# Performance work log

Hardware: AMD Instinct MI355X
Metric: run time of the kernel (lower is better)

Reference implementation:

```python
import jax, jax.numpy as jnp
import numpy as np

B, N, NE = 16, 96, 256
ATOM, EDIM, HID, LAT, HEADS = 128, 16, 128, 128, 4
HD = LAT // HEADS
RBF, CUT, ZEMB, MAXZ = 16, 5.0, 32, 100
MUL0_IN, MUL1_IN = 64, 32      # irreps_node = 64x0e + 32x1o (dim 160)
MUL0_OUT, MUL1_OUT = 32, 16    # out irreps  = 32x0e + 16x1o (dim 80)
NODE_DIM = MUL0_IN + 3 * MUL1_IN
OUT_DIM = MUL0_OUT + 3 * MUL1_OUT
E_ATT = 1024
WNUM = MUL0_IN*MUL0_OUT + MUL0_IN*MUL1_OUT + MUL1_IN*MUL1_OUT + MUL1_IN*MUL0_OUT  # 4608


def _mlp3(x, w1, b1, w2, b2, w3, b3):
    x = jax.nn.silu(x @ w1 + b1)
    x = jax.nn.silu(x @ w2 + b2)
    return x @ w3 + b3


def setup_inputs() -> dict:
    key = jax.random.key(0)
    ks = jax.random.split(key, 40)
    s = 0.05  # scale params so deep MLP activations stay numerically sane
    d = {}
    d['h'] = jax.random.normal(ks[0], (B, N, ATOM), jnp.float32)
    d['h_full'] = jax.random.normal(ks[1], (B, N, NODE_DIM), jnp.float32)
    d['e_feat'] = jax.random.normal(ks[2], (NE, EDIM), jnp.float32)
    d['att_dist'] = jax.random.uniform(ks[3], (E_ATT,), jnp.float32)
    d['att_vec'] = jax.random.normal(ks[4], (E_ATT, 3), jnp.float32)
    d['z_emb_table'] = jax.random.normal(ks[5], (MAXZ + 1, ZEMB), jnp.float32) * s
    d['rw1'] = jax.random.normal(ks[6], (ZEMB + 1 + RBF, HID), jnp.float32) * s
    d['rb1'] = jnp.zeros((HID,), jnp.float32)
    d['rw2'] = jax.random.normal(ks[7], (HID, WNUM), jnp.float32) * s
    d['rb2'] = jnp.zeros((WNUM,), jnp.float32)
    d['ew1'] = jax.random.normal(ks[8], (EDIM, HID), jnp.float32) * s
    d['eb1'] = jnp.zeros((HID,), jnp.float32)
    d['ew2'] = jax.random.normal(ks[9], (HID, MUL0_OUT + MUL1_OUT), jnp.float32) * s
    d['eb2'] = jnp.zeros((MUL0_OUT + MUL1_OUT,), jnp.float32)
    d['qw1'] = jax.random.normal(ks[10], (ATOM + EDIM, HID), jnp.float32) * s
    d['qb1'] = jnp.zeros((HID,), jnp.float32)
    d['qw2'] = jax.random.normal(ks[11], (HID, HID), jnp.float32) * s
    d['qb2'] = jnp.zeros((HID,), jnp.float32)
    d['qw3'] = jax.random.normal(ks[12], (HID, LAT), jnp.float32) * s
    d['qb3'] = jnp.zeros((LAT,), jnp.float32)
    d['kw1'] = jax.random.normal(ks[13], (ATOM + ZEMB + 1 + RBF, HID), jnp.float32) * s
    d['kb1'] = jnp.zeros((HID,), jnp.float32)
    d['kw2'] = jax.random.normal(ks[14], (HID, HID), jnp.float32) * s
    d['kb2'] = jnp.zeros((HID,), jnp.float32)
    d['kw3'] = jax.random.normal(ks[15], (HID, LAT), jnp.float32) * s
    d['kb3'] = jnp.zeros((LAT,), jnp.float32)
    d['ow1'] = jax.random.normal(ks[16], (MUL0_OUT + MUL1_OUT, HID), jnp.float32) * s
    d['ob1'] = jnp.zeros((HID,), jnp.float32)
    d['ow2'] = jax.random.normal(ks[17], (HID, HID), jnp.float32) * s
    d['ob2'] = jnp.zeros((HID,), jnp.float32)
    d['ow3'] = jax.random.normal(ks[18], (HID, LAT), jnp.float32) * s
    d['ob3'] = jnp.zeros((LAT,), jnp.float32)
    d['z'] = jax.random.randint(ks[19], (B, N), 0, MAXZ)
    d['mask'] = jnp.ones((B, N), bool)
    d['absorber_index'] = jax.random.randint(ks[20], (B,), 0, N)
    d['att_dst'] = jnp.arange(E_ATT)  # unique flat indices into B*N
    return d


def reference(h, h_full, e_feat, att_dist, att_vec, z_emb_table,
              rw1, rb1, rw2, rb2, ew1, eb1, ew2, eb2,
              qw1, qb1, qw2, qb2, qw3, qb3,
              kw1, kb1, kw2, kb2, kw3, kb3,
              ow1, ob1, ow2, ob2, ow3, ob3,
              z, mask, absorber_index, att_dst):
    Bz, Na, Hd = h.shape
    F = Bz * Na
    nE = e_feat.shape[0]
    # scatter edge data into flat (B*N) atom slots
    am_flat = jnp.zeros((F,), bool).at[att_dst].set(True)
    d_flat = jnp.zeros((F,), h.dtype).at[att_dst].set(att_dist)
    v_flat = jnp.zeros((F, 3), h.dtype).at[att_dst].set(att_vec)
    att_mask = am_flat.reshape(Bz, Na) & mask
    # spherical harmonics (lmax=1, component normalization): Y0 = 1, Y1 = sqrt(3)*unit_vec
    un = v_flat / jnp.maximum(jnp.linalg.norm(v_flat, axis=-1, keepdims=True), 1e-8)
    y1 = jnp.sqrt(3.0) * un
    # Gaussian RBF on absorber->atom distance
    mu = jnp.linspace(0.0, CUT, RBF)
    delta = CUT / (RBF - 1)
    rbf = jnp.exp(-(d_flat[:, None] - mu) ** 2 / (2.0 * delta * delta))  # (F, RBF)
    zr = z_emb_table[z]                      # (B, N, ZEMB)
    zr_flat = zr.reshape(F, -1)
    is_abs = jnp.zeros((Bz, Na), h.dtype).at[jnp.arange(Bz), absorber_index].set(1.0)
    # radial MLP -> per-edge tensor-product weights
    w_in = jnp.concatenate([zr_flat, is_abs.reshape(F, 1), rbf], -1)
    tpw = jax.nn.silu(w_in @ rw1 + rb1) @ rw2 + rb2  # (F, WNUM)
    s1 = MUL0_IN * MUL0_OUT
    s2 = s1 + MUL0_IN * MUL1_OUT
    s3 = s2 + MUL1_IN * MUL1_OUT
    w00 = tpw[:, :s1].reshape(F, MUL0_IN, MUL0_OUT)   # 0e x 0e -> 0e
    w01 = tpw[:, s1:s2].reshape(F, MUL0_IN, MUL1_OUT) # 0e x 1o -> 1o
    w10 = tpw[:, s2:s3].reshape(F, MUL1_IN, MUL1_OUT) # 1o x 0e -> 1o
    w11 = tpw[:, s3:].reshape(F, MUL1_IN, MUL0_OUT)   # 1o x 1o -> 0e
    hf = h_full.reshape(F, -1)
    x0 = hf[:, :MUL0_IN]
    x1 = hf[:, MUL0_IN:].reshape(F, MUL1_IN, 3)
    alpha = 1.0 / jnp.sqrt(jnp.float32(MUL0_IN + MUL1_IN))  # path fan-in normalization
    c = 1.0 / jnp.sqrt(3.0)                                  # wigner-3j coeff for l=1 couplings
    out0 = alpha * (jnp.einsum('fi,fio->fo', x0, w00)
                    + c * jnp.einsum('fim,fm,fio->fo', x1, y1, w11))
    out1 = alpha * c * (jnp.einsum('fi,fm,fio->fom', x0, y1, w01)
                        + jnp.einsum('fim,fio->fom', x1, w10))
    v_irrep = jnp.concatenate([out0, out1.reshape(F, 3 * MUL1_OUT)], -1)  # (F, OUT_DIM)
    # cosine cutoff envelope + edge mask
    env = jnp.where(d_flat < CUT, 0.5 * (jnp.cos(jnp.pi * d_flat / CUT) + 1.0), 0.0)
    v_irrep = v_irrep * (am_flat.astype(h.dtype) * env)[:, None]
    # energy-conditioned per-irrep-channel modulation
    gates = jax.nn.silu(e_feat @ ew1 + eb1) @ ew2 + eb2  # (nE, 48)
    g_exp = jnp.concatenate([gates[:, :MUL0_OUT],
                             jnp.repeat(gates[:, MUL0_OUT:], 3, axis=-1)], -1)  # (nE, OUT_DIM)
    v_mod = (v_irrep[:, None, :] * g_exp[None]).reshape(Bz, Na, nE, OUT_DIM)
    # invariant multi-head scoring
    h_abs = h[jnp.arange(Bz), absorber_index]  # (B, H)
    q_in = jnp.concatenate([jnp.broadcast_to(h_abs[:, None], (Bz, nE, Hd)),
                            jnp.broadcast_to(e_feat[None], (Bz, nE, EDIM))], -1)
    q = _mlp3(q_in, qw1, qb1, qw2, qb2, qw3, qb3)  # (B, nE, LAT)
    atom_static = jnp.concatenate([h, zr, is_abs[..., None], rbf.reshape(Bz, Na, RBF)], -1)
    k = _mlp3(atom_static, kw1, kb1, kw2, kb2, kw3, kb3)  # (B, N, LAT)
    qh = q.reshape(Bz, nE, HEADS, HD)
    kh = k.reshape(Bz, Na, HEADS, HD)
    scores = (jnp.einsum('behd,bnhd->benh', qh, kh) * (HD ** -0.5)).mean(-1)  # (B, nE, N)
    m = att_mask[:, None, :]
    scores = jnp.where(m, scores, -1e9)
    attn = jax.nn.softmax(scores, axis=2) * m.astype(h.dtype)
    attn = attn / jnp.maximum(attn.sum(2, keepdims=True), 1e-8)
    out_irrep = jnp.einsum('ben,bnec->bec', attn, v_mod)  # (B, nE, OUT_DIM)
    # invariants: scalars + vector norms
    scal = out_irrep[..., :MUL0_OUT]
    vec = out_irrep[..., MUL0_OUT:].reshape(Bz, nE, MUL1_OUT, 3)
    inv = jnp.concatenate([scal, jnp.sqrt(jnp.sum(vec * vec, -1) + 1e-12)], -1)
    return _mlp3(inv, ow1, ob1, ow2, ob2, ow3, ob3)  # (B, nE, LAT)
```

## Files before the change

### kernel.cpp

```cpp
#include <hip/hip_runtime.h>
#include <hip/hip_fp16.h>
#include <math.h>

#define BB 16
#define NN 96
#define NE 256
#define FF (BB*NN)
#define ATOM 128
#define EDIM 16
#define HID 128
#define LAT 128
#define RBFN 16
#define CUTOFF 5.0f
#define ZEMB 32
#define E_ATT 1024
#define M0I 64
#define M1I 32
#define M0O 32
#define M1O 16
#define NODE_DIM 160
#define OUT_DIM 80
#define INVD 48
#define WNUM 4608
#define SEG1 2048
#define SEG2 3072
#define SEG3 3584

#define NODE_BLKS (FF/4)
#define EC_BLKS 16
#define HABS_BLKS 2
#define GATE_BLKS 16
#define TRANS_BLKS 144
#define STAGE1_BLKS (NODE_BLKS + EC_BLKS + HABS_BLKS + GATE_BLKS + TRANS_BLKS)

#define MFMA_BLKS (36*16)
#define MQ_BLKS (MFMA_BLKS + 512)

typedef _Float16 half8_t __attribute__((ext_vector_type(8)));
typedef float float4v __attribute__((ext_vector_type(4)));

__device__ __forceinline__ float silu_f(float x) { return x / (1.0f + expf(-x)); }

__global__ __launch_bounds__(1024) void k_prep(
    const int* __restrict__ att_dst, const float* __restrict__ att_dist,
    const float* __restrict__ att_vec,
    int* __restrict__ inv, float* __restrict__ y1E, float* __restrict__ envE)
{
    int t = threadIdx.x;
    inv[t] = -1;
    if (t < FF - 1024) inv[1024 + t] = -1;
    {
        float d = att_dist[t];
        envE[t] = (d < CUTOFF) ? 0.5f*(cosf(3.14159265358979323846f*d/CUTOFF) + 1.0f) : 0.0f;
        float vx = att_vec[3*t], vy = att_vec[3*t+1], vz = att_vec[3*t+2];
        float nrm = sqrtf(vx*vx + vy*vy + vz*vz);
        float is = 1.0f / fmaxf(nrm, 1e-8f);
        const float s3 = 1.7320508075688772f;
        y1E[3*t]   = s3*vx*is;
        y1E[3*t+1] = s3*vy*is;
        y1E[3*t+2] = s3*vz*is;
    }
    __syncthreads();
    inv[att_dst[t]] = t;
}

__global__ __launch_bounds__(256) void k_stage1(
    const float* __restrict__ h, const float* __restrict__ z_emb, const int* __restrict__ z,
    const int* __restrict__ absorber, const float* __restrict__ e_feat,
    const int* __restrict__ inv, const float* __restrict__ att_dist,
    const float* __restrict__ rw1, const float* __restrict__ rb1,
    const float* __restrict__ kw1, const float* __restrict__ kb1,
    const float* __restrict__ kw2, const float* __restrict__ kb2,
    const float* __restrict__ kw3, const float* __restrict__ kb3,
    const float* __restrict__ qw1,
    const float* __restrict__ ew1, const float* __restrict__ eb1,
    const float* __restrict__ ew2, const float* __restrict__ eb2,
    const float* __restrict__ rw2,
    __half* __restrict__ hiddenH, float* __restrict__ kmatw,
    float* __restrict__ ecw, float* __restrict__ habs1w, float* __restrict__ gexp,
    __half* __restrict__ rw2T)
{
    __shared__ float smem[3488];
    int blk = blockIdx.x;
    int t = threadIdx.x;

    if (blk < NODE_BLKS) {
        float (*sin1)[184] = (float(*)[184])smem;
        float (*l1S)[128]  = (float(*)[128])(smem + 736);
        float (*l2S)[128]  = (float(*)[128])(smem + 736 + 512);
        int f0 = blk * 4;
        {
            int n = t >> 6, i2 = t & 63;
            float2 hv = *(const float2*)&h[(f0 + n)*ATOM + i2*2];
            sin1[n][i2*2] = hv.x; sin1[n][i2*2 + 1] = hv.y;
        }
        if (t < 128) {
            int n = t >> 5, j = t & 31;
            sin1[n][ATOM + j] = z_emb[z[f0 + n]*ZEMB + j];
        }
        if (t < 64) {
            int n = t >> 4, j = t & 15;
            int e = inv[f0 + n];
            float d = ((unsigned)e < E_ATT) ? att_dist[e] : 0.0f;
            const float delta = CUTOFF / (RBFN - 1);
            float diff = d - j*delta;
            sin1[n][ATOM + ZEMB + 1 + j] = expf(-diff*diff / (2.0f*delta*delta));
        }
        if (t < 4) {
            int f = f0 + t;
            int b = f / NN, nn = f - b*NN;
            sin1[t][ATOM + ZEMB] = (absorber[b] == nn) ? 1.0f : 0.0f;
        }
        __syncthreads();
        int n = t >> 6;
        int c2 = (t & 63) * 2;
        int e = inv[f0 + n];
        bool att_ = ((unsigned)e < E_ATT);
        if (att_) {
            float2 a0 = *(const float2*)&rb1[c2];
            float2 a1 = make_float2(0.f, 0.f);
            #pragma unroll 8
            for (int i = 0; i < 48; i += 2) {
                float x0v = sin1[n][ATOM + i], x1v = sin1[n][ATOM + i + 1];
                float2 w0 = *(const float2*)&rw1[i*HID + c2];
                float2 w1 = *(const float2*)&rw1[(i+1)*HID + c2];
                a0.x += x0v*w0.x; a0.y += x0v*w0.y;
                a1.x += x1v*w1.x; a1.y += x1v*w1.y;
            }
            {
                float x0v = sin1[n][ATOM + 48];
                float2 w0 = *(const float2*)&rw1[48*HID + c2];
                a0.x += x0v*w0.x; a0.y += x0v*w0.y;
            }
            *(__half2*)&hiddenH[e*HID + c2] =
                __floats2half2_rn(silu_f(a0.x + a1.x), silu_f(a0.y + a1.y));
        }
        {
            float2 a0 = *(const float2*)&kb1[c2];
            float2 a1 = make_float2(0.f, 0.f);
            #pragma unroll 8
            for (int i = 0; i < 176; i += 2) {
                float x0v = sin1[n][i], x1v = sin1[n][i + 1];
                float2 w0 = *(const float2*)&kw1[i*HID + c2];
                float2 w1 = *(const float2*)&kw1[(i+1)*HID + c2];
                a0.x += x0v*w0.x; a0.y += x0v*w0.y;
                a1.x += x1v*w1.x; a1.y += x1v*w1.y;
            }
            {
                float x0v = sin1[n][176];
                float2 w0 = *(const float2*)&kw1[176*HID + c2];
                a0.x += x0v*w0.x; a0.y += x0v*w0.y;
            }
            l1S[n][c2] = silu_f(a0.x + a1.x); l1S[n][c2+1] = silu_f(a0.y + a1.y);
        }
        __syncthreads();
        {
            float2 a0 = *(const float2*)&kb2[c2];
            float2 a1 = make_float2(0.f, 0.f);
            #pragma unroll 8
            for (int i = 0; i < HID; i += 2) {
                float x0v = l1S[n][i], x1v = l1S[n][i + 1];
                float2 w0 = *(const float2*)&kw2[i*HID + c2];
                float2 w1 = *(const float2*)&kw2[(i+1)*HID + c2];
                a0.x += x0v*w0.x; a0.y += x0v*w0.y;
                a1.x += x1v*w1.x; a1.y += x1v*w1.y;
            }
            l2S[n][c2] = silu_f(a0.x + a1.x); l2S[n][c2+1] = silu_f(a0.y + a1.y);
        }
        __syncthreads();
        {
            float2 a0 = *(const float2*)&kb3[c2];
            float2 a1 = make_float2(0.f, 0.f);
            #pragma unroll 8
            for (int i = 0; i < HID; i += 2) {
                float x0v = l2S[n][i], x1v = l2S[n][i + 1];
                float2 w0 = *(const float2*)&kw3[i*HID + c2];
                float2 w1 = *(const float2*)&kw3[(i+1)*HID + c2];
                a0.x += x0v*w0.x; a0.y += x0v*w0.y;
                a1.x += x1v*w1.x; a1.y += x1v*w1.y;
            }
            float2 o; o.x = a0.x + a1.x; o.y = a0.y + a1.y;
            *(float2*)&kmatw[(f0 + n)*HID + c2] = o;
        }
    } else if (blk < NODE_BLKS + EC_BLKS) {
        float (*ef)[16] = (float(*)[16])smem;
        int e0 = (blk - NODE_BLKS) * 16;
        { int e = t >> 4, i = t & 15; ef[e][i] = e_feat[(e0 + e)*EDIM + i]; }
        __syncthreads();
        int r = t >> 4, c0 = (t & 15)*8;
        float4 a0 = make_float4(0,0,0,0), a1 = a0;
        #pragma unroll
        for (int i = 0; i < EDIM; i++) {
            float a = ef[r][i];
            float4 w0 = *(const float4*)&qw1[(ATOM + i)*HID + c0];
            float4 w1 = *(const float4*)&qw1[(ATOM + i)*HID + c0 + 4];
            a0.x += a*w0.x; a0.y += a*w0.y; a0.z += a*w0.z; a0.w += a*w0.w;
            a1.x += a*w1.x; a1.y += a*w1.y; a1.z += a*w1.z; a1.w += a*w1.w;
        }
        *(float4*)&ecw[(e0 + r)*HID + c0] = a0;
        *(float4*)&ecw[(e0 + r)*HID + c0 + 4] = a1;
    } else if (blk < NODE_BLKS + EC_BLKS + HABS_BLKS) {
        float (*hr)[128] = (float(*)[128])smem;
        int b0 = (blk - NODE_BLKS - EC_BLKS) * 8;
        {
            int r = t >> 5, i4 = t & 31;
            int b = b0 + r;
            int a = absorber[b];
            *(float4*)&hr[r][i4*4] = *(const float4*)&h[(b*NN + a)*ATOM + i4*4];
        }
        __syncthreads();
        int r = t >> 5, c0 = (t & 31)*4;
        float4 a0 = make_float4(0,0,0,0), a1 = a0;
        #pragma unroll 8
        for (int i = 0; i < ATOM; i += 2) {
            float x0v = hr[r][i], x1v = hr[r][i+1];
            float4 w0 = *(const float4*)&qw1[i*HID + c0];
            float4 w1 = *(const float4*)&qw1[(i+1)*HID + c0];
            a0.x += x0v*w0.x; a0.y += x0v*w0.y; a0.z += x0v*w0.z; a0.w += x0v*w0.w;
            a1.x += x1v*w1.x; a1.y += x1v*w1.y; a1.z += x1v*w1.z; a1.w += x1v*w1.w;
        }
        float4 o;
        o.x = a0.x + a1.x; o.y = a0.y + a1.y; o.z = a0.z + a1.z; o.w = a0.w + a1.w;
        *(float4*)&habs1w[(b0 + r)*HID + c0] = o;
    } else if (blk < NODE_BLKS + EC_BLKS + HABS_BLKS + GATE_BLKS) {
        float (*ef)[16]   = (float(*)[16])smem;
        float (*l1g)[128] = (float(*)[128])(smem + 256);
        float (*gg)[48]   = (float(*)[48])(smem + 256 + 2048);
        int e0 = (blk - NODE_BLKS - EC_BLKS - HABS_BLKS) * 16;
        { int e = t >> 4, i = t & 15; ef[e][i] = e_feat[(e0 + e)*EDIM + i]; }
        __syncthreads();
        int r = t >> 4, c0 = (t & 15)*8;
        {
            float4 a0 = *(const float4*)&eb1[c0];
            float4 a1 = *(const float4*)&eb1[c0 + 4];
            #pragma unroll
            for (int i = 0; i < EDIM; i++) {
                float a = ef[r][i];
                float4 w0 = *(const float4*)&ew1[i*HID + c0];
                float4 w1 = *(const float4*)&ew1[i*HID + c0 + 4];
                a0.x += a*w0.x; a0.y += a*w0.y; a0.z += a*w0.z; a0.w += a*w0.w;
                a1.x += a*w1.x; a1.y += a*w1.y; a1.z += a*w1.z; a1.w += a*w1.w;
            }
            l1g[r][c0]   = silu_f(a0.x); l1g[r][c0+1] = silu_f(a0.y);
            l1g[r][c0+2] = silu_f(a0.z); l1g[r][c0+3] = silu_f(a0.w);
            l1g[r][c0+4] = silu_f(a1.x); l1g[r][c0+5] = silu_f(a1.y);
            l1g[r][c0+6] = silu_f(a1.z); l1g[r][c0+7] = silu_f(a1.w);
        }
        __syncthreads();
        for (int u = t; u < 16*48; u += 256) {
            int e = u / 48, j = u - 48*(u/48);
            float acc = eb2[j];
            #pragma unroll 4
            for (int i = 0; i < HID; i++) acc += l1g[e][i]*ew2[i*48 + j];
            gg[e][j] = acc;
        }
        __syncthreads();
        for (int u = t; u < 16*80; u += 256) {
            int e = u / 80, cc = u - 80*(u/80);
            gexp[(e0 + e)*OUT_DIM + cc] = (cc < M0O) ? gg[e][cc] : gg[e][M0O + (cc - M0O)/3];
        }
    } else {
        __half* lds = (__half*)smem;
        int tb = blk - (NODE_BLKS + EC_BLKS + HABS_BLKS + GATE_BLKS);
        int nt = tb % 72, kt = tb / 72;
        int n0 = nt*64, k0 = kt*64;
        for (int p = 0; p < 16; p++) {
            int idx = t + 256*p;
            int kk = idx >> 6, nn = idx & 63;
            lds[nn*66 + kk] = __float2half(rw2[(k0+kk)*WNUM + n0+nn]);
        }
        __syncthreads();
        for (int p = 0; p < 16; p++) {
            int idx = t + 256*p;
            int nn = idx >> 6, kk = idx & 63;
            rw2T[(n0+nn)*HID + k0+kk] = lds[nn*66 + kk];
        }
    }
}

__global__ __launch_bounds__(256) void k_mq(
    const __half* __restrict__ hiddenH, const __half* __restrict__ rw2T,
    const float* __restrict__ rb2,
    const float* __restrict__ habs1, const float* __restrict__ ec, const float* __restrict__ qb1,
    const float* __restrict__ qw2, const float* __restrict__ qb2,
    const float* __restrict__ qw3, const float* __restrict__ qb3,
    __half* __restrict__ tpwE, float* __restrict__ qmat)
{
    __shared__ __align__(16) char smemraw[17408];
    int blk = blockIdx.x;
    int t = threadIdx.x;
    if (blk < MFMA_BLKS) {
        int colTile = blk % 36;
        int rowGrp  = blk / 36;
        int wv = t >> 6;
        int lane = t & 63;
        int m0 = (rowGrp*4 + wv) * 16;
        int n0 = colTile * 128;
        int mrow = lane & 15, quad = lane >> 4;
        __half* cS = (__half*)smemraw + wv * (16*136);
        const _Float16* hp = (const _Float16*)hiddenH + (m0 + mrow)*HID + quad*8;
        half8_t af[4];
        #pragma unroll
        for (int kc = 0; kc < 4; kc++) af[kc] = *(const half8_t*)(hp + kc*32);
        #pragma unroll
        for (int nt = 0; nt < 8; nt++) {
            const _Float16* bp = (const _Float16*)rw2T + (n0 + nt*16 + mrow)*HID + quad*8;
            float4v acc = {0.f, 0.f, 0.f, 0.f};
            #pragma unroll
            for (int kc = 0; kc < 4; kc++) {
                half8_t bf = *(const half8_t*)(bp + kc*32);
                acc = __builtin_amdgcn_mfma_f32_16x16x32_f16(af[kc], bf, acc, 0, 0, 0);
            }
            float bias = rb2[n0 + nt*16 + mrow];
            #pragma unroll
            for (int r = 0; r < 4; r++)
                cS[(quad*4 + r)*136 + nt*16 + mrow] = __float2half(acc[r] + bias);
        }
        #pragma unroll
        for (int p = 0; p < 4; p++) {
            int chunk = lane + 64*p;
            int row = chunk >> 4, c8 = (chunk & 15)*8;
            float4 v = *(float4*)&cS[row*136 + c8];
            *(float4*)&tpwE[(long)(m0 + row)*WNUM + n0 + c8] = v;
        }
    } else {
        float* l1S = (float*)smemraw;
        float* l2S = (float*)smemraw + 1024;
        int r0 = (blk - MFMA_BLKS) * 8;
        for (int p = 0; p < 4; p++) {
            int idx = t + 256*p;
            int rr = idx >> 7, i = idx & 127;
            int be = r0 + rr; int b = be >> 8; int e = be & 255;
            l1S[rr*128 + i] = silu_f(habs1[b*HID + i] + ec[e*HID + i] + qb1[i]);
        }
        __syncthreads();
        int r = t >> 5, c0 = (t & 31)*4;
        {
            float4 a0 = *(const float4*)&qb2[c0];
            float4 a1 = make_float4(0,0,0,0);
            #pragma unroll 8
            for (int i = 0; i < HID; i += 2) {
                float x0v = l1S[r*128 + i], x1v = l1S[r*128 + i+1];
                float4 w0 = *(const float4*)&qw2[i*HID + c0];
                float4 w1 = *(const float4*)&qw2[(i+1)*HID + c0];
                a0.x += x0v*w0.x; a0.y += x0v*w0.y; a0.z += x0v*w0.z; a0.w += x0v*w0.w;
                a1.x += x1v*w1.x; a1.y += x1v*w1.y; a1.z += x1v*w1.z; a1.w += x1v*w1.w;
            }
            l2S[r*128 + c0]   = silu_f(a0.x + a1.x); l2S[r*128 + c0+1] = silu_f(a0.y + a1.y);
            l2S[r*128 + c0+2] = silu_f(a0.z + a1.z); l2S[r*128 + c0+3] = silu_f(a0.w + a1.w);
        }
        __syncthreads();
        {
            float4 a0 = *(const float4*)&qb3[c0];
            float4 a1 = make_float4(0,0,0,0);
            #pragma unroll 8
            for (int i = 0; i < HID; i += 2) {
                float x0v = l2S[r*128 + i], x1v = l2S[r*128 + i+1];
                float4 w0 = *(const float4*)&qw3[i*HID + c0];
                float4 w1 = *(const float4*)&qw3[(i+1)*HID + c0];
                a0.x += x0v*w0.x; a0.y += x0v*w0.y; a0.z += x0v*w0.z; a0.w += x0v*w0.w;
                a1.x += x1v*w1.x; a1.y += x1v*w1.y; a1.z += x1v*w1.z; a1.w += x1v*w1.w;
            }
            float4 o;
            o.x = a0.x + a1.x; o.y = a0.y + a1.y; o.z = a0.z + a1.z; o.w = a0.w + a1.w;
            *(float4*)&qmat[(r0 + r)*LAT + c0] = o;
        }
    }
}

__global__ __launch_bounds__(256) void k_score(
    const float* __restrict__ qmat, const float* __restrict__ kmat, const int* __restrict__ inv,
    float* __restrict__ scoresW)
{
    int b  = blockIdx.x >> 3;
    int e0 = (blockIdx.x & 7) * 32;
    int t = threadIdx.x;
    __shared__ float Qs[32][132];
    __shared__ float Ks[96][132];
    __shared__ float mS[NN];

    for (int p = 0; p < 4; p++) {
        int idx = t + 256*p; int e = idx >> 5, i4 = idx & 31;
        *(float4*)&Qs[e][i4*4] = *(const float4*)&qmat[(b*NE + e0 + e)*LAT + i4*4];
    }
    for (int p = 0; p < 12; p++) {
        int idx = t + 256*p; int n = idx >> 5, i4 = idx & 31;
        *(float4*)&Ks[n][i4*4] = *(const float4*)&kmat[(b*NN + n)*LAT + i4*4];
    }
    if (t < NN) mS[t] = ((unsigned)inv[b*NN + t] < E_ATT) ? 1.0f : 0.0f;
    __syncthreads();

    int te = t >> 5;
    int tn = t & 31;
    float acc[4][3] = {};
    for (int i = 0; i < LAT; i++) {
        float bv0 = Ks[tn][i], bv1 = Ks[tn + 32][i], bv2 = Ks[tn + 64][i];
        #pragma unroll
        for (int j = 0; j < 4; j++) {
            float a = Qs[te*4 + j][i];
            acc[j][0] += a*bv0; acc[j][1] += a*bv1; acc[j][2] += a*bv2;
        }
    }
    const float scale = 0.04419417382415922f;
    #pragma unroll
    for (int j = 0; j < 4; j++)
        #pragma unroll
        for (int jj = 0; jj < 3; jj++) {
            int n = tn + 32*jj;
            float s = (mS[n] != 0.f) ? acc[j][jj]*scale : -1e9f;
            scoresW[((b*NE) + e0 + te*4 + j)*NN + n] = s;
        }
}

__global__ __launch_bounds__(256) void k_tp(
    const float* __restrict__ h_full, const __half* __restrict__ tpwE,
    const int* __restrict__ att_dst,
    const float* __restrict__ envE, const float* __restrict__ y1E,
    float* __restrict__ virr)
{
    int t = threadIdx.x;
    int sub = t >> 7, tt = t & 127;
    int e = blockIdx.x*2 + sub;
    int f = att_dst[e];
    __shared__ float x0[2][M0I];
    __shared__ float x1f[2][M1I*3];
    __shared__ float xy[2][M1I];
    __shared__ float y1s[2][3];
    const float* hf = h_full + f*NODE_DIM;
    if (tt < M0I) x0[sub][tt] = hf[tt];
    if (tt < M1I*3) x1f[sub][tt] = hf[M0I + tt];
    if (tt < 3) y1s[sub][tt] = y1E[3*e + tt];
    __syncthreads();
    if (tt < M1I) xy[sub][tt] = x1f[sub][3*tt]*y1s[sub][0] + x1f[sub][3*tt+1]*y1s[sub][1]
                              + x1f[sub][3*tt+2]*y1s[sub][2];
    __syncthreads();
    float scale = envE[e];
    const __half* w = tpwE + (long)e*WNUM;
    const float alpha = 0.10206207261596575f;
    const float cc = 0.5773502691896258f;
    if (tt < M0O) {
        float t00 = 0.f, t11 = 0.f;
        #pragma unroll 4
        for (int i = 0; i < M0I; i++) t00 += x0[sub][i]*__half2float(w[i*M0O + tt]);
        #pragma unroll 4
        for (int i = 0; i < M1I; i++) t11 += xy[sub][i]*__half2float(w[SEG3 + i*M0O + tt]);
        virr[f*OUT_DIM + tt] = alpha*(t00 + cc*t11)*scale;
    } else if (tt < M0O + 3*M1O) {
        int idx = tt - M0O; int o = idx/3, m = idx - 3*o;
        float t01 = 0.f, t10 = 0.f;
        #pragma unroll 4
        for (int i = 0; i < M0I; i++) t01 += x0[sub][i]*__half2float(w[SEG1 + i*M1O + o]);
        #pragma unroll 4
        for (int i = 0; i < M1I; i++) t10 += x1f[sub][i*3 + m]*__half2float(w[SEG2 + i*M1O + o]);
        virr[f*OUT_DIM + tt] = alpha*cc*(t01*y1s[sub][m] + t10)*scale;
    }
}

__global__ __launch_bounds__(256) void k_attf(
    const float* __restrict__ scoresW, const int* __restrict__ inv,
    const float* __restrict__ virr, const float* __restrict__ gexp,
    const float* __restrict__ ow1, const float* __restrict__ ob1,
    const float* __restrict__ ow2, const float* __restrict__ ob2,
    const float* __restrict__ ow3, const float* __restrict__ ob3,
    float* __restrict__ out)
{
    int b  = blockIdx.x >> 5;
    int e0 = (blockIdx.x & 31) * 8;
    int t = threadIdx.x;
    __shared__ float aS[8][100];
    __shared__ float gS[8][84];
    __shared__ float ocS[8][84];
    __shared__ float mS[NN];
    __shared__ float inS[8][INVD];
    __shared__ float l1S[8][HID];
    __shared__ float l2S[8][HID];

    for (int p = 0; p < 3; p++) {
        int idx = t + 256*p;
        int el = idx / NN, n = idx - NN*(idx/NN);
        aS[el][n] = scoresW[((b*NE) + e0 + el)*NN + n];
    }
    if (t < 160) {
        int el = t / 20, c4 = t - 20*(t/20);
        *(float4*)&gS[el][c4*4] = *(const float4*)&gexp[(e0 + el)*OUT_DIM + c4*4];
    }
    if (t < NN) mS[t] = ((unsigned)inv[b*NN + t] < E_ATT) ? 1.0f : 0.0f;
    __syncthreads();

    {
        int el = t >> 5;
        int ng = t & 31;
        float s0 = aS[el][ng], s1 = aS[el][ng + 32], s2 = aS[el][ng + 64];
        float m0 = mS[ng], m1 = mS[ng + 32], m2 = mS[ng + 64];
        float mx = fmaxf(s0, fmaxf(s1, s2));
        #pragma unroll
        for (int off = 1; off < 32; off <<= 1) mx = fmaxf(mx, __shfl_xor(mx, off));
        float e0v = expf(s0 - mx), e1v = expf(s1 - mx), e2v = expf(s2 - mx);
        float sm = e0v + e1v + e2v;
        #pragma unroll
        for (int off = 1; off < 32; off <<= 1) sm += __shfl_xor(sm, off);
        float r = 1.0f / sm;
        float p0 = m0*e0v*r, p1 = m1*e1v*r, p2 = m2*e2v*r;
        float ss = p0 + p1 + p2;
        #pragma unroll
        for (int off = 1; off < 32; off <<= 1) ss += __shfl_xor(ss, off);
        float is = 1.0f / fmaxf(ss, 1e-8f);
        aS[el][ng]      = p0*is;
        aS[el][ng + 32] = p1*is;
        aS[el][ng + 64] = p2*is;
    }
    __syncthreads();

    if (t < 160) {
        int el = t / 20, c4 = t - 20*(t/20);
        const float* vp = virr + (long)b*NN*OUT_DIM + c4*4;
        float4 acc = make_float4(0,0,0,0);
        #pragma unroll 4
        for (int n = 0; n < NN; n++) {
            float a = aS[el][n];
            float4 v = *(const float4*)&vp[n*OUT_DIM];
            acc.x += a*v.x; acc.y += a*v.y; acc.z += a*v.z; acc.w += a*v.w;
        }
        float4 g = *(float4*)&gS[el][c4*4];
        float4 o; o.x = acc.x*g.x; o.y = acc.y*g.y; o.z = acc.z*g.z; o.w = acc.w*g.w;
        *(float4*)&ocS[el][c4*4] = o;
    }
    __syncthreads();

    for (int u = t; u < 8*INVD; u += 256) {
        int el = u / INVD, j = u - INVD*(u/INVD);
        float val;
        if (j < M0O) val = ocS[el][j];
        else {
            int o = j - M0O;
            float x = ocS[el][M0O + 3*o], y = ocS[el][M0O + 3*o + 1], zz = ocS[el][M0O + 3*o + 2];
            val = sqrtf(x*x + y*y + zz*zz + 1e-12f);
        }
        inS[el][j] = val;
    }
    __syncthreads();

    int r = t >> 5, c0 = (t & 31)*4;
    {
        float4 a0 = *(const float4*)&ob1[c0];
        float4 a1 = make_float4(0,0,0,0);
        #pragma unroll 8
        for (int i = 0; i < INVD; i += 2) {
            float x0v = inS[r][i], x1v = inS[r][i+1];
            float4 w0 = *(const float4*)&ow1[i*HID + c0];
            float4 w1 = *(const float4*)&ow1[(i+1)*HID + c0];
            a0.x += x0v*w0.x; a0.y += x0v*w0.y; a0.z += x0v*w0.z; a0.w += x0v*w0.w;
            a1.x += x1v*w1.x; a1.y += x1v*w1.y; a1.z += x1v*w1.z; a1.w += x1v*w1.w;
        }
        l1S[r][c0]   = silu_f(a0.x + a1.x); l1S[r][c0+1] = silu_f(a0.y + a1.y);
        l1S[r][c0+2] = silu_f(a0.z + a1.z); l1S[r][c0+3] = silu_f(a0.w + a1.w);
    }
    __syncthreads();
    {
        float4 a0 = *(const float4*)&ob2[c0];
        float4 a1 = make_float4(0,0,0,0);
        #pragma unroll 8
        for (int i = 0; i < HID; i += 2) {
            float x0v = l1S[r][i], x1v = l1S[r][i+1];
            float4 w0 = *(const float4*)&ow2[i*HID + c0];
            float4 w1 = *(const float4*)&ow2[(i+1)*HID + c0];
            a0.x += x0v*w0.x; a0.y += x0v*w0.y; a0.z += x0v*w0.z; a0.w += x0v*w0.w;
            a1.x += x1v*w1.x; a1.y += x1v*w1.y; a1.z += x1v*w1.z; a1.w += x1v*w1.w;
        }
        l2S[r][c0]   = silu_f(a0.x + a1.x); l2S[r][c0+1] = silu_f(a0.y + a1.y);
        l2S[r][c0+2] = silu_f(a0.z + a1.z); l2S[r][c0+3] = silu_f(a0.w + a1.w);
    }
    __syncthreads();
    {
        float4 a0 = *(const float4*)&ob3[c0];
        float4 a1 = make_float4(0,0,0,0);
        #pragma unroll 8
        for (int i = 0; i < HID; i += 2) {
            float x0v = l2S[r][i], x1v = l2S[r][i+1];
            float4 w0 = *(const float4*)&ow3[i*HID + c0];
            float4 w1 = *(const float4*)&ow3[(i+1)*HID + c0];
            a0.x += x0v*w0.x; a0.y += x0v*w0.y; a0.z += x0v*w0.z; a0.w += x0v*w0.w;
            a1.x += x1v*w1.x; a1.y += x1v*w1.y; a1.z += x1v*w1.z; a1.w += x1v*w1.w;
        }
        float4 o;
        o.x = a0.x + a1.x; o.y = a0.y + a1.y; o.z = a0.z + a1.z; o.w = a0.w + a1.w;
        *(float4*)&out[((b*NE + e0) + r)*LAT + c0] = o;
    }
}

extern "C" void kernel_launch(void* const* d_in, const int* in_sizes, int n_in,
                              void* d_out, int out_size, void* d_ws, size_t ws_size,
                              hipStream_t stream) {
    const float* h        = (const float*)d_in[0];
    const float* h_full   = (const float*)d_in[1];
    const float* e_feat   = (const float*)d_in[2];
    const float* att_dist = (const float*)d_in[3];
    const float* att_vec  = (const float*)d_in[4];
    const float* z_emb    = (const float*)d_in[5];
    const float* rw1 = (const float*)d_in[6];  const float* rb1 = (const float*)d_in[7];
    const float* rw2 = (const float*)d_in[8];  const float* rb2 = (const float*)d_in[9];
    const float* ew1 = (const float*)d_in[10]; const float* eb1 = (const float*)d_in[11];
    const float* ew2 = (const float*)d_in[12]; const float* eb2 = (const float*)d_in[13];
    const float* qw1 = (const float*)d_in[14]; const float* qb1 = (const float*)d_in[15];
    const float* qw2 = (const float*)d_in[16]; const float* qb2 = (const float*)d_in[17];
    const float* qw3 = (const float*)d_in[18]; const float* qb3 = (const float*)d_in[19];
    const float* kw1 = (const float*)d_in[20]; const float* kb1 = (const float*)d_in[21];
    const float* kw2 = (const float*)d_in[22]; const float* kb2 = (const float*)d_in[23];
    const float* kw3 = (const float*)d_in[24]; const float* kb3 = (const float*)d_in[25];
    const float* ow1 = (const float*)d_in[26]; const float* ob1 = (const float*)d_in[27];
    const float* ow2 = (const float*)d_in[28]; const float* ob2 = (const float*)d_in[29];
    const float* ow3 = (const float*)d_in[30]; const float* ob3 = (const float*)d_in[31];
    const int* z        = (const int*)d_in[32];
    const int* absorber = (const int*)d_in[34];
    const int* att_dst  = (const int*)d_in[35];

    float* ws = (float*)d_ws;
    int*   inv     = (int*)ws;
    float* y1E     = ws + 1536;
    float* envE    = ws + 4608;
    float* kmat    = ws + 5632;
    float* qmat    = ws + 202240;
    float* gexp    = ws + 726528;
    float* virr    = ws + 747008;
    float* habs1   = ws + 869888;
    float* ec      = ws + 871936;
    float* scoresW = ws + 904704;
    __half* tpwE   = (__half*)(ws + 1297920);
    __half* rw2T   = (__half*)(ws + 3657216);
    __half* hiddenH= (__half*)(ws + 3952128);

    float* out = (float*)d_out;

    k_prep<<<1, 1024, 0, stream>>>(att_dst, att_dist, att_vec, inv, y1E, envE);
    k_stage1<<<STAGE1_BLKS, 256, 0, stream>>>(h, z_emb, z, absorber, e_feat, inv, att_dist,
                                              rw1, rb1, kw1, kb1, kw2, kb2, kw3, kb3,
                                              qw1, ew1, eb1, ew2, eb2, rw2,
                                              hiddenH, kmat, ec, habs1, gexp, rw2T);
    k_mq<<<MQ_BLKS, 256, 0, stream>>>(hiddenH, rw2T, rb2, habs1, ec, qb1,
                                      qw2, qb2, qw3, qb3, tpwE, qmat);
    k_score<<<128, 256, 0, stream>>>(qmat, kmat, inv, scoresW);
    k_tp<<<E_ATT/2, 256, 0, stream>>>(h_full, tpwE, att_dst, envE, y1E, virr);
    k_attf<<<BB*32, 256, 0, stream>>>(scoresW, inv, virr, gexp,
                                      ow1, ob1, ow2, ob2, ow3, ob3, out);
}
```

Measured before the change: 248.4 us.

## Merge score and tensor-product kernels into one launch; skip K-MLP for unattended nodes

Combines k_score and k_tp into a single k_st launch with block-index dispatch, so one launch boundary disappears and the two independent workloads can share the GPU concurrently. The score path now streams K in three 32-row tiles through a shared buffer rather than holding all 96 rows, which shrinks LDS use. The K MLP layers in stage1 are guarded by `att_`, so nodes with no attention edge skip that work. Their kmat rows are left unwritten, which relies on the later masking to -1e9 making those rows irrelevant.

New measurement: 237.0 us. 4.6% less time.

```diff
diff --git a/kernel.cpp b/kernel.cpp
--- a/kernel.cpp
+++ b/kernel.cpp
@@ -36,6 +36,9 @@
 #define MFMA_BLKS (36*16)
 #define MQ_BLKS (MFMA_BLKS + 512)
 
+#define SCORE_BLKS 128
+#define ST_BLKS (SCORE_BLKS + 512)
+
 typedef _Float16 half8_t __attribute__((ext_vector_type(8)));
 typedef float float4v __attribute__((ext_vector_type(4)));
 
@@ -135,7 +138,7 @@
             *(__half2*)&hiddenH[e*HID + c2] =
                 __floats2half2_rn(silu_f(a0.x + a1.x), silu_f(a0.y + a1.y));
         }
-        {
+        if (att_) {
             float2 a0 = *(const float2*)&kb1[c2];
             float2 a1 = make_float2(0.f, 0.f);
             #pragma unroll 8
@@ -154,7 +157,7 @@
             l1S[n][c2] = silu_f(a0.x + a1.x); l1S[n][c2+1] = silu_f(a0.y + a1.y);
         }
         __syncthreads();
-        {
+        if (att_) {
             float2 a0 = *(const float2*)&kb2[c2];
             float2 a1 = make_float2(0.f, 0.f);
             #pragma unroll 8
@@ -168,7 +171,7 @@
             l2S[n][c2] = silu_f(a0.x + a1.x); l2S[n][c2+1] = silu_f(a0.y + a1.y);
         }
         __syncthreads();
-        {
+        if (att_) {
             float2 a0 = *(const float2*)&kb3[c2];
             float2 a1 = make_float2(0.f, 0.f);
             #pragma unroll 8
@@ -368,91 +371,88 @@
     }
 }
 
-__global__ __launch_bounds__(256) void k_score(
+__global__ __launch_bounds__(256) void k_st(
     const float* __restrict__ qmat, const float* __restrict__ kmat, const int* __restrict__ inv,
-    float* __restrict__ scoresW)
-{
-    int b  = blockIdx.x >> 3;
-    int e0 = (blockIdx.x & 7) * 32;
-    int t = threadIdx.x;
-    __shared__ float Qs[32][132];
-    __shared__ float Ks[96][132];
-    __shared__ float mS[NN];
-
-    for (int p = 0; p < 4; p++) {
-        int idx = t + 256*p; int e = idx >> 5, i4 = idx & 31;
-        *(float4*)&Qs[e][i4*4] = *(const float4*)&qmat[(b*NE + e0 + e)*LAT + i4*4];
-    }
-    for (int p = 0; p < 12; p++) {
-        int idx = t + 256*p; int n = idx >> 5, i4 = idx & 31;
-        *(float4*)&Ks[n][i4*4] = *(const float4*)&kmat[(b*NN + n)*LAT + i4*4];
-    }
-    if (t < NN) mS[t] = ((unsigned)inv[b*NN + t] < E_ATT) ? 1.0f : 0.0f;
-    __syncthreads();
-
-    int te = t >> 5;
-    int tn = t & 31;
-    float acc[4][3] = {};
-    for (int i = 0; i < LAT; i++) {
-        float bv0 = Ks[tn][i], bv1 = Ks[tn + 32][i], bv2 = Ks[tn + 64][i];
-        #pragma unroll
-        for (int j = 0; j < 4; j++) {
-            float a = Qs[te*4 + j][i];
-            acc[j][0] += a*bv0; acc[j][1] += a*bv1; acc[j][2] += a*bv2;
-        }
-    }
-    const float scale = 0.04419417382415922f;
-    #pragma unroll
-    for (int j = 0; j < 4; j++)
-        #pragma unroll
-        for (int jj = 0; jj < 3; jj++) {
-            int n = tn + 32*jj;
-            float s = (mS[n] != 0.f) ? acc[j][jj]*scale : -1e9f;
-            scoresW[((b*NE) + e0 + te*4 + j)*NN + n] = s;
-        }
-}
-
-__global__ __launch_bounds__(256) void k_tp(
     const float* __restrict__ h_full, const __half* __restrict__ tpwE,
     const int* __restrict__ att_dst,
     const float* __restrict__ envE, const float* __restrict__ y1E,
-    float* __restrict__ virr)
+    float* __restrict__ scoresW, float* __restrict__ virr)
 {
+    __shared__ float smem[8544];
+    int blk = blockIdx.x;
     int t = threadIdx.x;
-    int sub = t >> 7, tt = t & 127;
-    int e = blockIdx.x*2 + sub;
-    int f = att_dst[e];
-    __shared__ float x0[2][M0I];
-    __shared__ float x1f[2][M1I*3];
-    __shared__ float xy[2][M1I];
-    __shared__ float y1s[2][3];
-    const float* hf = h_full + f*NODE_DIM;
-    if (tt < M0I) x0[sub][tt] = hf[tt];
-    if (tt < M1I*3) x1f[sub][tt] = hf[M0I + tt];
-    if (tt < 3) y1s[sub][tt] = y1E[3*e + tt];
-    __syncthreads();
-    if (tt < M1I) xy[sub][tt] = x1f[sub][3*tt]*y1s[sub][0] + x1f[sub][3*tt+1]*y1s[sub][1]
-                              + x1f[sub][3*tt+2]*y1s[sub][2];
-    __syncthreads();
-    float scale = envE[e];
-    const __half* w = tpwE + (long)e*WNUM;
-    const float alpha = 0.10206207261596575f;
-    const float cc = 0.5773502691896258f;
-    if (tt < M0O) {
-        float t00 = 0.f, t11 = 0.f;
-        #pragma unroll 4
-        for (int i = 0; i < M0I; i++) t00 += x0[sub][i]*__half2float(w[i*M0O + tt]);
-        #pragma unroll 4
-        for (int i = 0; i < M1I; i++) t11 += xy[sub][i]*__half2float(w[SEG3 + i*M0O + tt]);
-        virr[f*OUT_DIM + tt] = alpha*(t00 + cc*t11)*scale;
-    } else if (tt < M0O + 3*M1O) {
-        int idx = tt - M0O; int o = idx/3, m = idx - 3*o;
-        float t01 = 0.f, t10 = 0.f;
-        #pragma unroll 4
-        for (int i = 0; i < M0I; i++) t01 += x0[sub][i]*__half2float(w[SEG1 + i*M1O + o]);
-        #pragma unroll 4
-        for (int i = 0; i < M1I; i++) t10 += x1f[sub][i*3 + m]*__half2float(w[SEG2 + i*M1O + o]);
-        virr[f*OUT_DIM + tt] = alpha*cc*(t01*y1s[sub][m] + t10)*scale;
+    if (blk < SCORE_BLKS) {
+        int b  = blk >> 3;
+        int e0 = (blk & 7) * 32;
+        float (*Qs)[132] = (float(*)[132])smem;
+        float (*Kt)[132] = (float(*)[132])(smem + 32*132);
+        float* mS = smem + 2*32*132;
+        for (int p = 0; p < 4; p++) {
+            int idx = t + 256*p; int e = idx >> 5, i4 = idx & 31;
+            *(float4*)&Qs[e][i4*4] = *(const float4*)&qmat[(b*NE + e0 + e)*LAT + i4*4];
+        }
+        if (t < NN) mS[t] = ((unsigned)inv[b*NN + t] < E_ATT) ? 1.0f : 0.0f;
+        int te = t >> 5, tn = t & 31;
+        float acc[4][3] = {};
+        for (int nt = 0; nt < 3; nt++) {
+            __syncthreads();
+            for (int p = 0; p < 4; p++) {
+                int idx = t + 256*p; int n = idx >> 5, i4 = idx & 31;
+                *(float4*)&Kt[n][i4*4] = *(const float4*)&kmat[(b*NN + nt*32 + n)*LAT + i4*4];
+            }
+            __syncthreads();
+            for (int i = 0; i < LAT; i++) {
+                float bv = Kt[tn][i];
+                acc[0][nt] += Qs[te*4 + 0][i]*bv;
+                acc[1][nt] += Qs[te*4 + 1][i]*bv;
+                acc[2][nt] += Qs[te*4 + 2][i]*bv;
+                acc[3][nt] += Qs[te*4 + 3][i]*bv;
+            }
+        }
+        const float scale = 0.04419417382415922f;
+        #pragma unroll
+        for (int j = 0; j < 4; j++)
+            #pragma unroll
+            for (int jj = 0; jj < 3; jj++) {
+                int n = tn + 32*jj;
+                float s = (mS[n] != 0.f) ? acc[j][jj]*scale : -1e9f;
+                scoresW[((b*NE) + e0 + te*4 + j)*NN + n] = s;
+            }
+    } else {
+        int sub = t >> 7, tt = t & 127;
+        int e = (blk - SCORE_BLKS)*2 + sub;
+        int f = att_dst[e];
+        float* x0  = smem + sub*256;
+        float* x1f = smem + sub*256 + 64;
+        float* xy  = smem + sub*256 + 160;
+        float* y1s = smem + sub*256 + 192;
+        const float* hf = h_full + f*NODE_DIM;
+        if (tt < M0I) x0[tt] = hf[tt];
+        if (tt < M1I*3) x1f[tt] = hf[M0I + tt];
+        if (tt < 3) y1s[tt] = y1E[3*e + tt];
+        __syncthreads();
+        if (tt < M1I) xy[tt] = x1f[3*tt]*y1s[0] + x1f[3*tt+1]*y1s[1] + x1f[3*tt+2]*y1s[2];
+        __syncthreads();
+        float scale = envE[e];
+        const __half* w = tpwE + (long)e*WNUM;
+        const float alpha = 0.10206207261596575f;
+        const float cc = 0.5773502691896258f;
+        if (tt < M0O) {
+            float t00 = 0.f, t11 = 0.f;
+            #pragma unroll 4
+            for (int i = 0; i < M0I; i++) t00 += x0[i]*__half2float(w[i*M0O + tt]);
+            #pragma unroll 4
+            for (int i = 0; i < M1I; i++) t11 += xy[i]*__half2float(w[SEG3 + i*M0O + tt]);
+            virr[f*OUT_DIM + tt] = alpha*(t00 + cc*t11)*scale;
+        } else if (tt < M0O + 3*M1O) {
+            int idx = tt - M0O; int o = idx/3, m = idx - 3*o;
+            float t01 = 0.f, t10 = 0.f;
+            #pragma unroll 4
+            for (int i = 0; i < M0I; i++) t01 += x0[i]*__half2float(w[SEG1 + i*M1O + o]);
+            #pragma unroll 4
+            for (int i = 0; i < M1I; i++) t10 += x1f[i*3 + m]*__half2float(w[SEG2 + i*M1O + o]);
+            virr[f*OUT_DIM + tt] = alpha*cc*(t01*y1s[m] + t10)*scale;
+        }
     }
 }
 
@@ -638,8 +638,8 @@
                                               hiddenH, kmat, ec, habs1, gexp, rw2T);
     k_mq<<<MQ_BLKS, 256, 0, stream>>>(hiddenH, rw2T, rb2, habs1, ec, qb1,
                                       qw2, qb2, qw3, qb3, tpwE, qmat);
-    k_score<<<128, 256, 0, stream>>>(qmat, kmat, inv, scoresW);
-    k_tp<<<E_ATT/2, 256, 0, stream>>>(h_full, tpwE, att_dst, envE, y1E, virr);
+    k_st<<<ST_BLKS, 256, 0, stream>>>(qmat, kmat, inv, h_full, tpwE, att_dst,
+                                      envE, y1E, scoresW, virr);
     k_attf<<<BB*32, 256, 0, stream>>>(scoresW, inv, virr, gexp,
                                       ow1, ob1, ow2, ob2, ow3, ob3, out);
 }
```
